# Kernel optimization log

Hardware: AMD Instinct MI355X
Metric: run time of the kernel (lower is better)

Reference implementation:

```python
import jax, jax.numpy as jnp
import numpy as np

NUM_HEADS = 4
LN_EPS = 1e-5


def setup_inputs() -> dict:
    key = jax.random.key(0)
    ks = jax.random.split(key, 12)
    B, S, D = 8, 2048, 256
    Dh = D // NUM_HEADS
    s = 0.02
    return {
        "descriptors": jax.random.normal(ks[0], (B, S, D), jnp.float32),
        # cached rotary embedding (cos, sin) pair broadcastable over heads
        "keypoints": jax.random.normal(ks[1], (2, B, 1, S, Dh), jnp.float32),
        "Wqkv_w": jax.random.normal(ks[2], (3 * D, D), jnp.float32) * s,
        "Wqkv_b": jax.random.normal(ks[3], (3 * D,), jnp.float32) * s,
        "Wo_w": jax.random.normal(ks[4], (D, D), jnp.float32) * s,
        "Wo_b": jax.random.normal(ks[5], (D,), jnp.float32) * s,
        "W1_w": jax.random.normal(ks[6], (2 * D, 2 * D), jnp.float32) * s,
        "W1_b": jax.random.normal(ks[7], (2 * D,), jnp.float32) * s,
        "ln_g": jnp.ones((2 * D,), jnp.float32),
        "ln_b": jnp.zeros((2 * D,), jnp.float32),
        "W2_w": jax.random.normal(ks[8], (D, 2 * D), jnp.float32) * s,
        "W2_b": jax.random.normal(ks[9], (D,), jnp.float32) * s,
    }


def _rotate_half(x):
    # pairwise rotation: (x0,x1,x2,x3,...) -> (-x1,x0,-x3,x2,...)
    xr = x.reshape(x.shape[:-1] + (x.shape[-1] // 2, 2))
    return jnp.stack((-xr[..., 1], xr[..., 0]), axis=-1).reshape(x.shape)


def reference(descriptors, keypoints, Wqkv_w, Wqkv_b, Wo_w, Wo_b,
              W1_w, W1_b, ln_g, ln_b, W2_w, W2_b):
    B, S, D = descriptors.shape
    H = NUM_HEADS
    Dh = D // H
    # fused QKV projection; torch layout: last dim = (H, Dh, 3) interleaved
    qkv = descriptors @ Wqkv_w.T + Wqkv_b           # [B,S,3D]
    qkv = qkv.reshape(B, S, H, Dh, 3).transpose(0, 2, 1, 3, 4)  # [B,H,S,Dh,3]
    q, k, v = qkv[..., 0], qkv[..., 1], qkv[..., 2]
    # rotary embedding on q, k
    cos, sin = keypoints[0], keypoints[1]           # [B,1,S,Dh]
    q = q * cos + _rotate_half(q) * sin
    k = k * cos + _rotate_half(k) * sin
    # scaled dot-product attention
    scale = jnp.float32(Dh) ** -0.5
    sim = jnp.einsum('bhid,bhjd->bhij', q, k) * scale
    attn = jax.nn.softmax(sim, axis=-1)
    ctx = jnp.einsum('bhij,bhjd->bhid', attn, v)    # [B,H,S,Dh]
    ctx = ctx.transpose(0, 2, 1, 3).reshape(B, S, D)
    message = ctx @ Wo_w.T + Wo_b
    # FFN over concat(descriptors, message)
    x = jnp.concatenate([descriptors, message], axis=-1)  # [B,S,2D]
    x = x @ W1_w.T + W1_b
    mu = jnp.mean(x, axis=-1, keepdims=True)
    var = jnp.var(x, axis=-1, keepdims=True)
    x = (x - mu) * jax.lax.rsqrt(var + LN_EPS) * ln_g + ln_b
    x = jax.nn.gelu(x, approximate=False)
    x = x @ W2_w.T + W2_b
    return descriptors + x
```

## Files before the change

### kernel.cpp

```cpp
#include <hip/hip_runtime.h>
#include <math.h>

#define B_  8
#define S_  2048
#define D_  256
#define H_  4
#define DH  64
#define M_  (B_ * S_)
#define QS  4194304

typedef __attribute__((ext_vector_type(8))) short bf16x8;
typedef __attribute__((ext_vector_type(4))) float f32x4;
typedef unsigned short u16;
typedef unsigned int   u32;

#define AS1 __attribute__((address_space(1)))
#define AS3 __attribute__((address_space(3)))

__device__ __forceinline__ u16 f2bf(float x) {
    union { float f; u32 u; } c; c.f = x;
    u32 r = (c.u + 0x7fffu + ((c.u >> 16) & 1u)) >> 16;
    return (u16)r;
}
__device__ __forceinline__ float bf2f(u16 x) {
    union { u32 u; float f; } c; c.u = ((u32)x) << 16;
    return c.f;
}

__device__ __forceinline__ void gload16(const void* g, void* l) {
    __builtin_amdgcn_global_load_lds((const AS1 unsigned int*)g,
                                     (AS3 unsigned int*)l, 16, 0, 0);
}

__global__ __launch_bounds__(256) void cast7_kernel(
    const float* __restrict__ desc, u16* __restrict__ descb,
    const float* __restrict__ wqkv, u16* __restrict__ wqkvb,
    const float* __restrict__ wo,   const float* __restrict__ w1,
    u16* __restrict__ w1f,
    const float* __restrict__ w2,   u16* __restrict__ w2b,
    const float* __restrict__ w1_b, const float* __restrict__ wo_b,
    float* __restrict__ bias1f)
{
    int bid = blockIdx.x;
    const int tid = threadIdx.x;

    if (bid >= 5184) {
        const int row = bid - 5184;
        const int col = tid;
        const float* wrow = w1 + (size_t)row * 512 + 256;
        float acc = 0.f;
#pragma unroll 4
        for (int k = 0; k < 256; k++)
            acc += wrow[k] * wo[(size_t)k * 256 + col];
        w1f[(size_t)row * 512 + 256 + col] = f2bf(acc);
        return;
    }
    if (bid >= 4672) {
        __shared__ float red[4];
        const int n = bid - 4672;
        float p = w1[(size_t)n * 512 + 256 + tid] * wo_b[tid];
#pragma unroll
        for (int off = 1; off < 64; off <<= 1) p += __shfl_xor(p, off);
        if ((tid & 63) == 0) red[tid >> 6] = p;
        __syncthreads();
        if (tid == 0) bias1f[n] = red[0] + red[1] + red[2] + red[3] + w1_b[n];
        return;
    }
    if (bid >= 4544) {
        const int i = ((bid - 4544) * 256 + tid) * 4;
        const float4 v = *(const float4*)(w2 + i);
        u16 o[4] = {f2bf(v.x), f2bf(v.y), f2bf(v.z), f2bf(v.w)};
        *(uint2*)(w2b + i) = *(const uint2*)o;
        return;
    }
    if (bid >= 4288) {
        const int e = ((bid - 4288) * 256 + tid) * 4;
        const int row = e >> 9, col = e & 511;
        if (col < 256) {
            const float4 v = *(const float4*)(w1 + e);
            u16 o[4] = {f2bf(v.x), f2bf(v.y), f2bf(v.z), f2bf(v.w)};
            *(uint2*)(w1f + (size_t)row * 512 + col) = *(const uint2*)o;
        }
        return;
    }
    const float* s; u16* d;
    if (bid < 4096) { s = desc; d = descb; }
    else            { s = wqkv; d = wqkvb; bid -= 4096; }
    const int i = (bid * 256 + tid) * 4;
    const float4 v = *(const float4*)(s + i);
    u16 o[4] = {f2bf(v.x), f2bf(v.y), f2bf(v.z), f2bf(v.w)};
    *(uint2*)(d + i) = *(const uint2*)o;
}

template <int NT, int CONCAT, int RES, int OUTBF16>
__global__ __launch_bounds__(256) void gemm_bf16(
    const u16* __restrict__ A, const u16* __restrict__ A2,
    const u16* __restrict__ W, const float* __restrict__ bias,
    const float* __restrict__ res, float* __restrict__ Cf,
    u16* __restrict__ Cb, int K, int N, int ldc)
{
    __shared__ u16 As[128 * 64];
    __shared__ u16 Bs[NT * 32 * 64];
    const int tid  = threadIdx.x;
    const int w    = tid >> 6;
    const int lane = tid & 63;
    const int n    = lane & 15;
    const int quad = lane >> 4;
    const int m0   = blockIdx.x * 128;
    const int n0   = blockIdx.y * (NT * 32);
    const int m_off = (w >> 1) * 64;
    const int n_off = (w & 1) * (NT * 16);
    const int lrow = lane >> 3;
    const int lcol = (lane & 7) * 8;

    f32x4 acc[4][NT];
#pragma unroll
    for (int i = 0; i < 4; i++)
#pragma unroll
        for (int j = 0; j < NT; j++) acc[i][j] = (f32x4){0.f, 0.f, 0.f, 0.f};

    for (int k0 = 0; k0 < K; k0 += 64) {
        const u16* Asrc;
        int kb, lda;
        if (CONCAT) { Asrc = (k0 < 256) ? A : A2; kb = k0 & 255; lda = 256; }
        else        { Asrc = A; kb = k0; lda = K; }

        __syncthreads();
#pragma unroll
        for (int it = 0; it < 4; it++) {
            const int r0 = it * 32 + w * 8;
            gload16(Asrc + (size_t)(m0 + r0 + lrow) * lda + kb + lcol, &As[r0 * 64]);
        }
#pragma unroll
        for (int it = 0; it < NT; it++) {
            const int r0 = it * 32 + w * 8;
            gload16(W + (size_t)(n0 + r0 + lrow) * K + k0 + lcol, &Bs[r0 * 64]);
        }
        __syncthreads();

        bf16x8 af[4][2], bf[NT][2];
#pragma unroll
        for (int mt = 0; mt < 4; mt++)
#pragma unroll
            for (int t = 0; t < 2; t++)
                af[mt][t] = *(const bf16x8*)&As[(m_off + mt * 16 + n) * 64 + t * 32 + quad * 8];
#pragma unroll
        for (int nt = 0; nt < NT; nt++)
#pragma unroll
            for (int t = 0; t < 2; t++)
                bf[nt][t] = *(const bf16x8*)&Bs[(n_off + nt * 16 + n) * 64 + t * 32 + quad * 8];

#pragma unroll
        for (int mt = 0; mt < 4; mt++)
#pragma unroll
            for (int nt = 0; nt < NT; nt++) {
                acc[mt][nt] = __builtin_amdgcn_mfma_f32_16x16x32_bf16(af[mt][0], bf[nt][0], acc[mt][nt], 0, 0, 0);
                acc[mt][nt] = __builtin_amdgcn_mfma_f32_16x16x32_bf16(af[mt][1], bf[nt][1], acc[mt][nt], 0, 0, 0);
            }
    }

#pragma unroll
    for (int nt = 0; nt < NT; nt++) {
        const int col = n0 + n_off + nt * 16 + n;
        const float bv = bias[col];
#pragma unroll
        for (int mt = 0; mt < 4; mt++) {
#pragma unroll
            for (int r = 0; r < 4; r++) {
                const int row = m0 + m_off + mt * 16 + quad * 4 + r;
                float o = acc[mt][nt][r] + bv;
                if (RES) o += res[(size_t)row * ldc + col];
                if (OUTBF16) Cb[(size_t)row * ldc + col] = f2bf(o);
                else         Cf[(size_t)row * ldc + col] = o;
            }
        }
    }
}

#define QSCALE 0.18033688011112042f

__global__ __launch_bounds__(256) void ropevt_kernel(
    const u16* __restrict__ qkv, const float* __restrict__ kp,
    u16* __restrict__ q, u16* __restrict__ k, u16* __restrict__ vt)
{
    __shared__ u32 vbuf[32 * 128];

    const int bh = blockIdx.x;
    const int s0 = blockIdx.y * 128;
    const int b  = bh >> 2;
    const int h  = bh & 3;
    const int t  = threadIdx.x;
    const int dp = t & 31;
    const int d  = dp * 2;

    const size_t qkbase = ((size_t)bh * S_ + s0) * DH;
#pragma unroll
    for (int i = 0; i < 16; i++) {
        const int sl = i * 8 + (t >> 5);
        const int s  = s0 + sl;
        const u16* src = qkv + (size_t)(b * S_ + s) * 768 + h * 192 + dp * 6;
        const u32 w0 = *(const u32*)(src);
        const u32 w1 = *(const u32*)(src + 2);
        const u32 w2 = *(const u32*)(src + 4);
        const float qe = bf2f((u16)w0), ke = bf2f((u16)(w0 >> 16));
        const float qo = bf2f((u16)(w1 >> 16));
        const float ko = bf2f((u16)w2);

        const size_t kidx = ((size_t)b * S_ + s) * DH + d;
        const float2 cs = *(const float2*)(kp + kidx);
        const float2 sn = *(const float2*)(kp + (size_t)B_ * S_ * DH + kidx);

        const float qe2 = (qe * cs.x - qo * sn.x) * QSCALE;
        const float qo2 = (qo * cs.y + qe * sn.y) * QSCALE;
        const float ke2 = ke * cs.x - ko * sn.x;
        const float ko2 = ko * cs.y + ke * sn.y;

        const size_t oidx = qkbase + (size_t)sl * DH + d;
        *(u32*)(q + oidx) = (u32)f2bf(qe2) | ((u32)f2bf(qo2) << 16);
        *(u32*)(k + oidx) = (u32)f2bf(ke2) | ((u32)f2bf(ko2) << 16);
        vbuf[dp * 128 + (sl ^ dp)] = (w1 & 0xffffu) | (w2 & 0xffff0000u);
    }
    __syncthreads();

    u16* vtp = vt + (size_t)bh * DH * S_ + s0;
#pragma unroll
    for (int i = 0; i < 16; i++) {
        const int dd  = i * 4 + (t >> 6);
        const int sp  = t & 63;
        const int dpr = dd >> 1;
        const u32 a = vbuf[dpr * 128 + ((2 * sp)     ^ dpr)];
        const u32 c = vbuf[dpr * 128 + ((2 * sp + 1) ^ dpr)];
        const u32 o = (dd & 1) ? ((a >> 16)      | (c & 0xffff0000u))
                               : ((a & 0xffffu)  | (c << 16));
        *(u32*)(vtp + (size_t)dd * S_ + 2 * sp) = o;
    }
}

#define NEG12L2E -17.312340490667562f

__global__ __launch_bounds__(256, 2) void attn_kernel(
    const u16* __restrict__ q, const u16* __restrict__ k,
    const u16* __restrict__ vt, u16* __restrict__ ctx)
{
    __shared__ u16 ks[128 * 64];
    __shared__ u16 vs[64 * 128];
    __shared__ u16 ps[128 * 128];

    const int tid  = threadIdx.x;
    const int w    = tid >> 6;
    const int lane = tid & 63;
    const int n    = lane & 15;
    const int quad = lane >> 4;
    const int lrow = lane >> 3;
    const int vrow = lane >> 4;
    const int bh   = blockIdx.x;
    const int q0   = blockIdx.y * 128;
    const int nsw  = n & 7;

    const int kcol  = (((lane & 7) ^ lrow) * 8);
    const int vcol0 = (((lane & 15) ^ vrow) * 8);
    const int vcol1 = (((lane & 15) ^ (4 + vrow)) * 8);

    const u16* qbase = q  + (size_t)bh * S_ * DH;
    const u16* kbase = k  + (size_t)bh * S_ * DH;
    const u16* vbase = vt + (size_t)bh * DH * S_;
    const int b    = bh >> 2;
    const int h    = bh & 3;

    bf16x8 qf[2][2];
#pragma unroll
    for (int mb = 0; mb < 2; mb++)
#pragma unroll
        for (int t = 0; t < 2; t++)
            qf[mb][t] = *(const bf16x8*)(qbase +
                (size_t)(q0 + w * 32 + mb * 16 + n) * DH + (t * 4 + quad) * 8);

    f32x4 o[2][4];
#pragma unroll
    for (int mb = 0; mb < 2; mb++)
#pragma unroll
        for (int j = 0; j < 4; j++) o[mb][j] = (f32x4){0.f, 0.f, 0.f, 0.f};
    float lrun[2] = {0.f, 0.f};

    for (int kb = 0; kb < S_ / 128; kb++) {
        const int k0 = kb * 128;
        __syncthreads();
#pragma unroll
        for (int it = 0; it < 4; it++) {
            const int r0 = w * 32 + it * 8;
            gload16(kbase + (size_t)(k0 + r0 + lrow) * DH + kcol, &ks[r0 * 64]);
            const int d0 = w * 16 + it * 4;
            gload16(vbase + (size_t)(d0 + vrow) * S_ + k0 + ((it & 1) ? vcol1 : vcol0),
                    &vs[d0 * 128]);
        }
        __syncthreads();

        f32x4 sacc[2][8];
#pragma unroll
        for (int mb = 0; mb < 2; mb++)
#pragma unroll
            for (int j = 0; j < 8; j++)
                sacc[mb][j] = (f32x4){NEG12L2E, NEG12L2E, NEG12L2E, NEG12L2E};
        __builtin_amdgcn_s_setprio(1);
#pragma unroll
        for (int t = 0; t < 2; t++) {
#pragma unroll
            for (int j = 0; j < 8; j++) {
                const bf16x8 kf = *(const bf16x8*)
                    &ks[(16 * j + n) * 64 + (((t * 4 + quad) ^ nsw) * 8)];
                sacc[0][j] = __builtin_amdgcn_mfma_f32_16x16x32_bf16(kf, qf[0][t], sacc[0][j], 0, 0, 0);
                sacc[1][j] = __builtin_amdgcn_mfma_f32_16x16x32_bf16(kf, qf[1][t], sacc[1][j], 0, 0, 0);
            }
        }
        __builtin_amdgcn_s_setprio(0);

#pragma unroll
        for (int mb = 0; mb < 2; mb++) {
            float rs = 0.f;
            const int prow = (w * 32 + mb * 16 + n) * 128;
#pragma unroll
            for (int j = 0; j < 8; j++) {
                const float e0 = __builtin_amdgcn_exp2f(sacc[mb][j][0]);
                const float e1 = __builtin_amdgcn_exp2f(sacc[mb][j][1]);
                const float e2 = __builtin_amdgcn_exp2f(sacc[mb][j][2]);
                const float e3 = __builtin_amdgcn_exp2f(sacc[mb][j][3]);
                rs += (e0 + e1) + (e2 + e3);
                uint2 pk;
                pk.x = (u32)f2bf(e0) | ((u32)f2bf(e1) << 16);
                pk.y = (u32)f2bf(e2) | ((u32)f2bf(e3) << 16);
                const int blk = (4 * j + quad) ^ (nsw << 2);
                *(uint2*)&ps[prow + blk * 4] = pk;
            }
            lrun[mb] += rs;
        }

        __builtin_amdgcn_s_setprio(1);
#pragma unroll
        for (int kt = 0; kt < 4; kt++) {
            const bf16x8 pf0 = *(const bf16x8*)
                &ps[(w * 32 +      n) * 128 + ((32 * kt + 8 * quad) ^ (nsw << 4))];
            const bf16x8 pf1 = *(const bf16x8*)
                &ps[(w * 32 + 16 + n) * 128 + ((32 * kt + 8 * quad) ^ (nsw << 4))];
#pragma unroll
            for (int nt = 0; nt < 4; nt++) {
                const bf16x8 vf = *(const bf16x8*)
                    &vs[(16 * nt + n) * 128 + (((kt * 4 + quad) ^ nsw) * 8)];
                o[0][nt] = __builtin_amdgcn_mfma_f32_16x16x32_bf16(pf0, vf, o[0][nt], 0, 0, 0);
                o[1][nt] = __builtin_amdgcn_mfma_f32_16x16x32_bf16(pf1, vf, o[1][nt], 0, 0, 0);
            }
        }
        __builtin_amdgcn_s_setprio(0);
    }

#pragma unroll
    for (int mb = 0; mb < 2; mb++) {
        float s = lrun[mb];
        s += __shfl_xor(s, 16);
        s += __shfl_xor(s, 32);
        lrun[mb] = s;
    }

#pragma unroll
    for (int mb = 0; mb < 2; mb++) {
#pragma unroll
        for (int r = 0; r < 4; r++) {
            const float sv = __shfl(lrun[mb], quad * 4 + r);
            const float inv = 1.f / sv;
            const int row = q0 + w * 32 + mb * 16 + quad * 4 + r;
#pragma unroll
            for (int nt = 0; nt < 4; nt++)
                ctx[((size_t)b * S_ + row) * D_ + h * DH + 16 * nt + n] = f2bf(o[mb][nt][r] * inv);
        }
    }
}

__global__ __launch_bounds__(256) void ln_gelu_kernel(
    const u16* __restrict__ x, const float* __restrict__ g,
    const float* __restrict__ bt, u16* __restrict__ y)
{
    const int m    = blockIdx.x * 4 + (threadIdx.x >> 6);
    const int lane = threadIdx.x & 63;
    const int c0   = lane * 8;
    uint4 xv = *(const uint4*)(x + (size_t)m * 512 + c0);
    const u16* xp = (const u16*)&xv;
    float v[8];
    float s = 0.f, sq = 0.f;
#pragma unroll
    for (int j = 0; j < 8; j++) {
        v[j] = bf2f(xp[j]);
        s  += v[j];
        sq += v[j] * v[j];
    }
#pragma unroll
    for (int off = 1; off < 64; off <<= 1) {
        s  += __shfl_xor(s, off);
        sq += __shfl_xor(sq, off);
    }
    const float mu   = s * (1.f / 512.f);
    const float var  = sq * (1.f / 512.f) - mu * mu;
    const float rstd = rsqrtf(var + 1e-5f);

    const float4 g0 = *(const float4*)(g  + c0);
    const float4 g1 = *(const float4*)(g  + c0 + 4);
    const float4 b0 = *(const float4*)(bt + c0);
    const float4 b1 = *(const float4*)(bt + c0 + 4);
    const float gg[8] = {g0.x, g0.y, g0.z, g0.w, g1.x, g1.y, g1.z, g1.w};
    const float bb[8] = {b0.x, b0.y, b0.z, b0.w, b1.x, b1.y, b1.z, b1.w};
    u16 o[8];
#pragma unroll
    for (int j = 0; j < 8; j++) {
        const float yj = (v[j] - mu) * rstd * gg[j] + bb[j];
        o[j] = f2bf(0.5f * yj * (1.f + erff(yj * 0.70710678118654752f)));
    }
    *(uint4*)(y + (size_t)m * 512 + c0) = *(const uint4*)o;
}

extern "C" void kernel_launch(void* const* d_in, const int* in_sizes, int n_in,
                              void* d_out, int out_size, void* d_ws, size_t ws_size,
                              hipStream_t stream)
{
    const float* desc   = (const float*)d_in[0];
    const float* kp     = (const float*)d_in[1];
    const float* Wqkv_w = (const float*)d_in[2];
    const float* Wqkv_b = (const float*)d_in[3];
    const float* Wo_w   = (const float*)d_in[4];
    const float* Wo_b   = (const float*)d_in[5];
    const float* W1_w   = (const float*)d_in[6];
    const float* W1_b   = (const float*)d_in[7];
    const float* ln_g   = (const float*)d_in[8];
    const float* ln_b   = (const float*)d_in[9];
    const float* W2_w   = (const float*)d_in[10];
    const float* W2_b   = (const float*)d_in[11];
    float* out = (float*)d_out;
    float* ws  = (float*)d_ws;

    u16*   qkvb  = (u16*)ws;
    u16*   x1b   = (u16*)(ws + 2 * (size_t)QS);
    u16*   qb    = (u16*)(ws + 3 * (size_t)QS);
    u16*   kb    = (u16*)(ws + (size_t)(3.5 * QS));
    u16*   x1g   = qb;
    u16*   ctxb  = (u16*)(ws + (size_t)(4.5 * QS));
    u16*   descb = (u16*)(ws + 5 * (size_t)QS);
    float* bias1f = ws + (size_t)(5.5 * QS);
    u16*   wpool = (u16*)(ws + 6 * (size_t)QS);
    u16*   vtb   = (u16*)(ws + (size_t)(6.5 * QS));
    u16* wqkvb = wpool;
    u16* w2b   = wqkvb + 196608;
    u16* w1f   = w2b   + 131072;

    const dim3 blk(256);

    cast7_kernel<<<dim3(5696), blk, 0, stream>>>(
        desc, descb, Wqkv_w, wqkvb, Wo_w, W1_w, w1f, W2_w, w2b,
        W1_b, Wo_b, bias1f);

    gemm_bf16<4, 0, 0, 1><<<dim3(M_ / 128, 768 / 128), blk, 0, stream>>>(
        descb, nullptr, wqkvb, Wqkv_b, nullptr, nullptr, qkvb, 256, 768, 768);

    ropevt_kernel<<<dim3(B_ * H_, S_ / 128), blk, 0, stream>>>(
        qkvb, kp, qb, kb, vtb);

    attn_kernel<<<dim3(B_ * H_, S_ / 128), blk, 0, stream>>>(qb, kb, vtb, ctxb);

    gemm_bf16<4, 1, 0, 1><<<dim3(M_ / 128, 512 / 128), blk, 0, stream>>>(
        descb, ctxb, w1f, bias1f, nullptr, nullptr, x1b, 512, 512, 512);

    ln_gelu_kernel<<<dim3(M_ / 4), blk, 0, stream>>>(x1b, ln_g, ln_b, x1g);

    gemm_bf16<2, 0, 1, 0><<<dim3(M_ / 128, 256 / 64), blk, 0, stream>>>(
        x1g, nullptr, w2b, W2_b, desc, out, nullptr, 512, 256, 256);
}
```

Baseline: 238.6 us.

## Double-buffer K tiles and split V wait to overlap loads with compute

The attention kernel now double-buffers the K tile in shared memory and prefetches the next K block while the current one is processed. V loads are issued at the top of each iteration, and the wait on them is deferred until after the QK^T and softmax stage using explicit vmcnt waits and raw barriers. The goal is to hide global-to-LDS latency behind MFMA and exp work. The cost is an extra 16KB of LDS, which may reduce occupancy, plus hand-counted vmcnt values that must match the number of outstanding loads.

```diff
diff --git a/kernel.cpp b/kernel.cpp
--- a/kernel.cpp
+++ b/kernel.cpp
@@ -242,9 +242,11 @@
     const u16* __restrict__ q, const u16* __restrict__ k,
     const u16* __restrict__ vt, u16* __restrict__ ctx)
 {
-    __shared__ u16 ks[128 * 64];
-    __shared__ u16 vs[64 * 128];
-    __shared__ u16 ps[128 * 128];
+    __shared__ u16 pool[40960];
+    u16* ks0 = pool;
+    u16* ks1 = pool + 8192;
+    u16* vs  = pool + 16384;
+    u16* ps  = pool + 24576;
 
     const int tid  = threadIdx.x;
     const int w    = tid >> 6;
@@ -275,6 +277,12 @@
             qf[mb][t] = *(const bf16x8*)(qbase +
                 (size_t)(q0 + w * 32 + mb * 16 + n) * DH + (t * 4 + quad) * 8);
 
+#pragma unroll
+    for (int it = 0; it < 4; it++) {
+        const int r0 = w * 32 + it * 8;
+        gload16(kbase + (size_t)(r0 + lrow) * DH + kcol, &ks0[r0 * 64]);
+    }
+
     f32x4 o[2][4];
 #pragma unroll
     for (int mb = 0; mb < 2; mb++)
@@ -284,16 +292,30 @@
 
     for (int kb = 0; kb < S_ / 128; kb++) {
         const int k0 = kb * 128;
-        __syncthreads();
+        u16* kcur = (kb & 1) ? ks1 : ks0;
+        u16* knxt = (kb & 1) ? ks0 : ks1;
+
+        asm volatile("" ::: "memory");
+        __builtin_amdgcn_s_barrier();
+
 #pragma unroll
         for (int it = 0; it < 4; it++) {
-            const int r0 = w * 32 + it * 8;
-            gload16(kbase + (size_t)(k0 + r0 + lrow) * DH + kcol, &ks[r0 * 64]);
             const int d0 = w * 16 + it * 4;
             gload16(vbase + (size_t)(d0 + vrow) * S_ + k0 + ((it & 1) ? vcol1 : vcol0),
                     &vs[d0 * 128]);
         }
-        __syncthreads();
+        if (kb < S_ / 128 - 1) {
+#pragma unroll
+            for (int it = 0; it < 4; it++) {
+                const int r0 = w * 32 + it * 8;
+                gload16(kbase + (size_t)(k0 + 128 + r0 + lrow) * DH + kcol,
+                        &knxt[r0 * 64]);
+            }
+            asm volatile("s_waitcnt vmcnt(8)" ::: "memory");
+        } else {
+            asm volatile("s_waitcnt vmcnt(4)" ::: "memory");
+        }
+        __builtin_amdgcn_s_barrier();
 
         f32x4 sacc[2][8];
 #pragma unroll
@@ -307,7 +329,7 @@
 #pragma unroll
             for (int j = 0; j < 8; j++) {
                 const bf16x8 kf = *(const bf16x8*)
-                    &ks[(16 * j + n) * 64 + (((t * 4 + quad) ^ nsw) * 8)];
+                    &kcur[(16 * j + n) * 64 + (((t * 4 + quad) ^ nsw) * 8)];
                 sacc[0][j] = __builtin_amdgcn_mfma_f32_16x16x32_bf16(kf, qf[0][t], sacc[0][j], 0, 0, 0);
                 sacc[1][j] = __builtin_amdgcn_mfma_f32_16x16x32_bf16(kf, qf[1][t], sacc[1][j], 0, 0, 0);
             }
@@ -333,6 +355,10 @@
             }
             lrun[mb] += rs;
         }
+
+        if (kb < S_ / 128 - 1) asm volatile("s_waitcnt vmcnt(4)" ::: "memory");
+        else                   asm volatile("s_waitcnt vmcnt(0)" ::: "memory");
+        __builtin_amdgcn_s_barrier();
 
         __builtin_amdgcn_s_setprio(1);
 #pragma unroll
```

Result: no change. 235.2 us (-1.4%).
